# Performance work log

Hardware: AMD Instinct MI355X
Metric: run time of the kernel (lower is better)

Reference implementation:

```python
import jax, jax.numpy as jnp
import numpy as np

N, D, H = 8192, 1280, 16
K = D // H          # head_dim = 80
S = 16              # number of packed segments
L = N // S          # tokens per segment = 512
SCALE = K ** -0.5


def rotate_half(x):
    x1, x2 = jnp.split(x, 2, axis=-1)
    return jnp.concatenate([-x2, x1], axis=-1)


def setup_inputs() -> dict:
    key = jax.random.key(0)
    ks = jax.random.split(key, 4)
    # RoPE tables over head_dim, shared by all heads
    inv_freq = 1.0 / (10000.0 ** (jnp.arange(0, K, 2, dtype=jnp.float32) / K))
    freqs = jnp.outer(jnp.arange(N, dtype=jnp.float32), inv_freq)  # [N, K/2]
    emb = jnp.concatenate([freqs, freqs], axis=-1)                 # [N, K]
    return {
        "hidden_ND": jax.random.normal(ks[0], (N, D), jnp.float32),
        "cu_seqlens": jnp.arange(S + 1, dtype=jnp.int32) * L,      # equal-length segments
        "cos_NK": jnp.cos(emb),
        "sin_NK": jnp.sin(emb),
        "qkv_w": jax.random.normal(ks[1], (D, 3 * D), jnp.float32) * (D ** -0.5),
        "qkv_b": jnp.zeros((3 * D,), jnp.float32),
        "proj_w": jax.random.normal(ks[2], (D, D), jnp.float32) * (D ** -0.5),
        "proj_b": jnp.zeros((D,), jnp.float32),
    }


def reference(hidden_ND, cu_seqlens, cos_NK, sin_NK, qkv_w, qkv_b, proj_w, proj_b):
    n = hidden_ND.shape[0]
    qkv = (hidden_ND @ qkv_w + qkv_b).reshape(n, 3, H, K)
    q, k, v = qkv[:, 0], qkv[:, 1], qkv[:, 2]          # each [N, H, K]
    cos = cos_NK[:, None, :]
    sin = sin_NK[:, None, :]
    q = q * cos + rotate_half(q) * sin
    k = k * cos + rotate_half(k) * sin
    # Block-diagonal attention over equal-length segments defined by cu_seqlens.
    num_seqs = cu_seqlens.shape[0] - 1
    seg_len = n // num_seqs
    qs = q.reshape(num_seqs, seg_len, H, K)
    ks_ = k.reshape(num_seqs, seg_len, H, K)
    vs = v.reshape(num_seqs, seg_len, H, K)
    logits = jnp.einsum('slhk,smhk->shlm', qs, ks_) * SCALE   # [S, H, L, L]
    w = jax.nn.softmax(logits.astype(jnp.float32), axis=-1).astype(logits.dtype)
    out = jnp.einsum('shlm,smhk->slhk', w, vs).reshape(n, H * K)
    return out @ proj_w + proj_b
```

## Files before the change

### kernel.cpp

```cpp
#include <hip/hip_runtime.h>

#define LOG2E 1.44269504088896340736f
#define ATT_SCALE 0.11180339887498949f

typedef _Float16 half8 __attribute__((ext_vector_type(8)));
typedef _Float16 half4v __attribute__((ext_vector_type(4)));
typedef float f32x4 __attribute__((ext_vector_type(4)));

#define MFMA(a, b, c) __builtin_amdgcn_mfma_f32_16x16x32_f16((a), (b), (c), 0, 0, 0)

__device__ __forceinline__ void async16(const _Float16* g, _Float16* l) {
  __builtin_amdgcn_global_load_lds(
      (const __attribute__((address_space(1))) unsigned int*)g,
      (__attribute__((address_space(3))) unsigned int*)l,
      16, 0, 0);
}

__global__ __launch_bounds__(256) void cvt_k(const float* __restrict__ in,
                                             _Float16* __restrict__ out, int n4) {
  int i = blockIdx.x * 256 + threadIdx.x;
  if (i < n4) {
    f32x4 v = ((const f32x4*)in)[i];
    half4v hv;
    hv[0] = (_Float16)v[0]; hv[1] = (_Float16)v[1];
    hv[2] = (_Float16)v[2]; hv[3] = (_Float16)v[3];
    ((half4v*)out)[i] = hv;
  }
}

__global__ __launch_bounds__(256) void transpose_cvt_k(const float* __restrict__ in,
                                                       _Float16* __restrict__ out,
                                                       int R, int C) {
  __shared__ float tile[32][33];
  const int tx = threadIdx.x & 31, ty = threadIdx.x >> 5;
  const int c0 = blockIdx.x * 32, r0 = blockIdx.y * 32;
#pragma unroll
  for (int i = 0; i < 32; i += 8)
    tile[ty + i][tx] = in[(size_t)(r0 + ty + i) * C + c0 + tx];
  __syncthreads();
#pragma unroll
  for (int i = 0; i < 32; i += 8)
    out[(size_t)(c0 + ty + i) * R + r0 + tx] = (_Float16)tile[tx][ty + i];
}

template <int MODE>
__global__ __launch_bounds__(256) void gemm_k(const _Float16* __restrict__ A,
                                              const _Float16* __restrict__ BT,
                                              const float* __restrict__ bias,
                                              _Float16* __restrict__ Qf,
                                              _Float16* __restrict__ Kf,
                                              _Float16* __restrict__ VTf,
                                              float* __restrict__ Out) {
  __shared__ _Float16 sA[128 * 64];
  __shared__ _Float16 sB[128 * 64];
  const int tid = threadIdx.x;
  const int wave = tid >> 6, lane = tid & 63;
  const int quad = lane >> 4, l16 = lane & 15;
  const int m0 = blockIdx.x * 128;
  const int n0 = blockIdx.y * 128;
  const int mw = (wave & 1) * 64, nw = (wave >> 1) * 64;
  const int KD = 1280;

  f32x4 acc[4][4] = {};

  for (int kt = 0; kt < KD; kt += 64) {
#pragma unroll
    for (int c = 0; c < 4; ++c) {
      const int j = wave * 4 + c;
      const int row = j * 8 + (lane >> 3);
      const int srcg = (lane & 7) ^ (row & 7);
      async16(A + (size_t)(m0 + row) * KD + kt + srcg * 8, &sA[j * 512]);
      async16(BT + (size_t)(n0 + row) * KD + kt + srcg * 8, &sB[j * 512]);
    }
    __syncthreads();
#pragma unroll
    for (int ks = 0; ks < 2; ++ks) {
      half8 af[4], bf[4];
#pragma unroll
      for (int i = 0; i < 4; ++i) {
        const int ra = mw + i * 16 + l16;
        const int rb = nw + i * 16 + l16;
        af[i] = *(const half8*)&sA[ra * 64 + (((ks * 4 + quad) ^ (ra & 7)) * 8)];
        bf[i] = *(const half8*)&sB[rb * 64 + (((ks * 4 + quad) ^ (rb & 7)) * 8)];
      }
#pragma unroll
      for (int i = 0; i < 4; ++i)
#pragma unroll
        for (int j2 = 0; j2 < 4; ++j2)
          acc[i][j2] = MFMA(af[i], bf[j2], acc[i][j2]);
    }
    __syncthreads();
  }

#pragma unroll
  for (int i = 0; i < 4; ++i) {
#pragma unroll
    for (int j2 = 0; j2 < 4; ++j2) {
      const int col = n0 + nw + j2 * 16 + l16;
      const float bv = bias[col];
      const int rowb = m0 + mw + i * 16 + quad * 4;
#pragma unroll
      for (int r = 0; r < 4; ++r) {
        const float v = acc[i][j2][r] + bv;
        const int mrow = rowb + r;
        if (MODE == 0) {
          const int which = col / 1280;
          const int rem = col - which * 1280;
          const int h = rem / 80;
          const int kk = rem - h * 80;
          const int s = mrow >> 9, l = mrow & 511;
          const int shh = s * 16 + h;
          if (which == 0)
            Qf[((size_t)shh * 512 + l) * 96 + kk] = (_Float16)v;
          else if (which == 1)
            Kf[((size_t)shh * 512 + l) * 96 + kk] = (_Float16)v;
          else
            VTf[((size_t)shh * 80 + kk) * 512 + l] = (_Float16)v;
        } else {
          Out[(size_t)mrow * 1280 + col] = v;
        }
      }
    }
  }
}

__global__ __launch_bounds__(256) void rope_k(_Float16* __restrict__ Qf,
                                              _Float16* __restrict__ Kf,
                                              const float* __restrict__ cosNK,
                                              const float* __restrict__ sinNK) {
  const int gid = blockIdx.x * 256 + threadIdx.x;
  const int j = gid & 63;
  const int row = gid >> 6;
  const int qk = row >> 17;
  const int r = row & 131071;
  _Float16* buf = qk ? Kf : Qf;
  const int l = r & 511;
  const int s = r >> 13;
  const int t = s * 512 + l;
  const size_t base = (size_t)r * 96;
  if (j < 40) {
    const float v1 = (float)buf[base + j];
    const float v2 = (float)buf[base + j + 40];
    const float c1 = cosNK[t * 80 + j], s1 = sinNK[t * 80 + j];
    const float c2 = cosNK[t * 80 + j + 40], s2 = sinNK[t * 80 + j + 40];
    buf[base + j] = (_Float16)(v1 * c1 - v2 * s1);
    buf[base + j + 40] = (_Float16)(v2 * c2 + v1 * s2);
  } else if (j < 56) {
    buf[base + 40 + j] = (_Float16)0.f;
  }
}

__global__ __launch_bounds__(256) void attn_k(const _Float16* __restrict__ Qf,
                                              const _Float16* __restrict__ Kf,
                                              const _Float16* __restrict__ VTf,
                                              _Float16* __restrict__ attnA) {
  __shared__ _Float16 sQP[128 * 96];
  __shared__ _Float16 sK[64 * 96];
  __shared__ _Float16 sV[96 * 72];
  const int tid = threadIdx.x;
  const int wave = tid >> 6, lane = tid & 63;
  const int quad = lane >> 4, l16 = lane & 15;
  const int shh = blockIdx.x;
  const int qt = blockIdx.y;
  const int h = shh & 15;
  const int s = shh >> 4;

  const _Float16* Qb = Qf + ((size_t)shh * 512 + qt * 128) * 96;
  const _Float16* Kb0 = Kf + (size_t)shh * 512 * 96;
  const _Float16* Vb0 = VTf + (size_t)shh * 80 * 512;

#pragma unroll
  for (int c = 0; c < 6; ++c) {
    const int j = wave + 4 * c;
    async16(Qb + j * 512 + lane * 8, &sQP[j * 512]);
  }
  for (int idx = tid; idx < 16 * 72; idx += 256) sV[80 * 72 + idx] = (_Float16)1.f;
  __syncthreads();

  const _Float16 c1h = (_Float16)(ATT_SCALE * LOG2E);
  half8 qf[2][3];
#pragma unroll
  for (int rt = 0; rt < 2; ++rt)
#pragma unroll
    for (int ks = 0; ks < 3; ++ks) {
      half8 t = *(const half8*)&sQP[(wave * 32 + rt * 16 + l16) * 96 + ks * 32 + quad * 8];
#pragma unroll
      for (int e = 0; e < 8; ++e) t[e] *= c1h;
      qf[rt][ks] = t;
    }

  f32x4 o[2][6] = {};

  for (int kc = 0; kc < 8; ++kc) {
    __syncthreads();
    const _Float16* Kb = Kb0 + (size_t)kc * 64 * 96;
#pragma unroll
    for (int c = 0; c < 3; ++c) {
      const int j = wave + 4 * c;
      async16(Kb + j * 512 + lane * 8, &sK[j * 512]);
    }
#pragma unroll
    for (int c = 0; c < 3; ++c) {
      const int j = wave + 4 * c;
      const int off = j * 1024 + lane * 16;
      const int vrow = off / 144;
      const int colb = off - vrow * 144;
      if (vrow < 80 && colb < 128)
        async16(Vb0 + (size_t)vrow * 512 + kc * 64 + (colb >> 1), &sV[j * 512]);
    }
    __syncthreads();

    f32x4 sacc[2][4] = {};
#pragma unroll
    for (int nt = 0; nt < 4; ++nt) {
#pragma unroll
      for (int ks = 0; ks < 3; ++ks) {
        half8 kb = *(const half8*)&sK[(nt * 16 + l16) * 96 + ks * 32 + quad * 8];
        sacc[0][nt] = MFMA(qf[0][ks], kb, sacc[0][nt]);
        sacc[1][nt] = MFMA(qf[1][ks], kb, sacc[1][nt]);
      }
    }

    _Float16* sP = sQP;
#pragma unroll
    for (int rt = 0; rt < 2; ++rt)
#pragma unroll
      for (int nt = 0; nt < 4; ++nt)
#pragma unroll
        for (int r = 0; r < 4; ++r)
          sP[(wave * 32 + rt * 16 + quad * 4 + r) * 72 + nt * 16 + l16] =
              (_Float16)__builtin_amdgcn_exp2f(sacc[rt][nt][r]);

#pragma unroll
    for (int ks = 0; ks < 2; ++ks) {
      half8 pa[2];
      pa[0] = *(const half8*)&sP[(wave * 32 + 0 + l16) * 72 + ks * 32 + quad * 8];
      pa[1] = *(const half8*)&sP[(wave * 32 + 16 + l16) * 72 + ks * 32 + quad * 8];
#pragma unroll
      for (int ft = 0; ft < 6; ++ft) {
        half8 vb = *(const half8*)&sV[(ft * 16 + l16) * 72 + ks * 32 + quad * 8];
        o[0][ft] = MFMA(pa[0], vb, o[0][ft]);
        o[1][ft] = MFMA(pa[1], vb, o[1][ft]);
      }
    }
  }

#pragma unroll
  for (int rt = 0; rt < 2; ++rt) {
#pragma unroll
    for (int r = 0; r < 4; ++r) {
      const float inv = 1.0f / o[rt][5][r];
      const int token = s * 512 + qt * 128 + wave * 32 + rt * 16 + quad * 4 + r;
#pragma unroll
      for (int ft = 0; ft < 5; ++ft)
        attnA[(size_t)token * 1280 + h * 80 + ft * 16 + l16] =
            (_Float16)(o[rt][ft][r] * inv);
    }
  }
}

extern "C" void kernel_launch(void* const* d_in, const int* in_sizes, int n_in,
                              void* d_out, int out_size, void* d_ws, size_t ws_size,
                              hipStream_t stream) {
  (void)in_sizes; (void)n_in; (void)out_size; (void)ws_size;
  const float* hidden = (const float*)d_in[0];
  const float* cosNK = (const float*)d_in[2];
  const float* sinNK = (const float*)d_in[3];
  const float* qkv_w = (const float*)d_in[4];
  const float* qkv_b = (const float*)d_in[5];
  const float* proj_w = (const float*)d_in[6];
  const float* proj_b = (const float*)d_in[7];
  float* out = (float*)d_out;

  char* ws = (char*)d_ws;
  _Float16* hA    = (_Float16*)(ws);
  _Float16* wT    = (_Float16*)(ws + 20971520);
  _Float16* projT = (_Float16*)(ws + 30801920);
  _Float16* Qf    = (_Float16*)(ws + 34078720);
  _Float16* Kf    = (_Float16*)(ws + 59244544);
  _Float16* VTf   = (_Float16*)(ws + 84410368);
  _Float16* attnA = (_Float16*)(ws + 105381888);

  cvt_k<<<10240, 256, 0, stream>>>(hidden, hA, 2621440);
  transpose_cvt_k<<<dim3(120, 40), 256, 0, stream>>>(qkv_w, wT, 1280, 3840);
  transpose_cvt_k<<<dim3(40, 40), 256, 0, stream>>>(proj_w, projT, 1280, 1280);
  gemm_k<0><<<dim3(64, 30), 256, 0, stream>>>(hA, wT, qkv_b, Qf, Kf, VTf, nullptr);
  rope_k<<<65536, 256, 0, stream>>>(Qf, Kf, cosNK, sinNK);
  attn_k<<<dim3(256, 4), 256, 0, stream>>>(Qf, Kf, VTf, attnA);
  gemm_k<1><<<dim3(64, 10), 256, 0, stream>>>(attnA, projT, proj_b, nullptr, nullptr,
                                              nullptr, out);
}
```

Measured before the change: 389.9 us.

## Shrink GEMM k-tile, pad K smem, transpose QK^T and pack P stores

```diff
diff --git a/kernel.cpp b/kernel.cpp
--- a/kernel.cpp
+++ b/kernel.cpp
@@ -5,6 +5,7 @@
 
 typedef _Float16 half8 __attribute__((ext_vector_type(8)));
 typedef _Float16 half4v __attribute__((ext_vector_type(4)));
+typedef __fp16 fp16x2 __attribute__((ext_vector_type(2)));
 typedef float f32x4 __attribute__((ext_vector_type(4)));
 
 #define MFMA(a, b, c) __builtin_amdgcn_mfma_f32_16x16x32_f16((a), (b), (c), 0, 0, 0)
@@ -51,8 +52,8 @@
                                               _Float16* __restrict__ Kf,
                                               _Float16* __restrict__ VTf,
                                               float* __restrict__ Out) {
-  __shared__ _Float16 sA[128 * 64];
-  __shared__ _Float16 sB[128 * 64];
+  __shared__ _Float16 sA[128 * 32];
+  __shared__ _Float16 sB[128 * 32];
   const int tid = threadIdx.x;
   const int wave = tid >> 6, lane = tid & 63;
   const int quad = lane >> 4, l16 = lane & 15;
@@ -61,34 +62,31 @@
   const int mw = (wave & 1) * 64, nw = (wave >> 1) * 64;
   const int KD = 1280;
 
+  const int srcg = (lane & 3) ^ ((lane >> 3) & 3);
+  const int rg = (quad ^ ((l16 >> 1) & 3)) * 8;
+
   f32x4 acc[4][4] = {};
 
-  for (int kt = 0; kt < KD; kt += 64) {
-#pragma unroll
-    for (int c = 0; c < 4; ++c) {
-      const int j = wave * 4 + c;
-      const int row = j * 8 + (lane >> 3);
-      const int srcg = (lane & 7) ^ (row & 7);
+  for (int kt = 0; kt < KD; kt += 32) {
+#pragma unroll
+    for (int c = 0; c < 2; ++c) {
+      const int j = wave * 2 + c;
+      const int row = j * 16 + (lane >> 2);
       async16(A + (size_t)(m0 + row) * KD + kt + srcg * 8, &sA[j * 512]);
       async16(BT + (size_t)(n0 + row) * KD + kt + srcg * 8, &sB[j * 512]);
     }
     __syncthreads();
-#pragma unroll
-    for (int ks = 0; ks < 2; ++ks) {
-      half8 af[4], bf[4];
-#pragma unroll
-      for (int i = 0; i < 4; ++i) {
-        const int ra = mw + i * 16 + l16;
-        const int rb = nw + i * 16 + l16;
-        af[i] = *(const half8*)&sA[ra * 64 + (((ks * 4 + quad) ^ (ra & 7)) * 8)];
-        bf[i] = *(const half8*)&sB[rb * 64 + (((ks * 4 + quad) ^ (rb & 7)) * 8)];
-      }
-#pragma unroll
-      for (int i = 0; i < 4; ++i)
-#pragma unroll
-        for (int j2 = 0; j2 < 4; ++j2)
-          acc[i][j2] = MFMA(af[i], bf[j2], acc[i][j2]);
-    }
+    half8 af[4], bf[4];
+#pragma unroll
+    for (int i = 0; i < 4; ++i) {
+      af[i] = *(const half8*)&sA[(mw + i * 16 + l16) * 32 + rg];
+      bf[i] = *(const half8*)&sB[(nw + i * 16 + l16) * 32 + rg];
+    }
+#pragma unroll
+    for (int i = 0; i < 4; ++i)
+#pragma unroll
+      for (int j2 = 0; j2 < 4; ++j2)
+        acc[i][j2] = MFMA(af[i], bf[j2], acc[i][j2]);
     __syncthreads();
   }
 
@@ -154,8 +152,8 @@
                                               const _Float16* __restrict__ Kf,
                                               const _Float16* __restrict__ VTf,
                                               _Float16* __restrict__ attnA) {
-  __shared__ _Float16 sQP[128 * 96];
-  __shared__ _Float16 sK[64 * 96];
+  __shared__ _Float16 sP[128 * 72];
+  __shared__ _Float16 sK[64 * 104];
   __shared__ _Float16 sV[96 * 72];
   const int tid = threadIdx.x;
   const int wave = tid >> 6, lane = tid & 63;
@@ -169,35 +167,36 @@
   const _Float16* Kb0 = Kf + (size_t)shh * 512 * 96;
   const _Float16* Vb0 = VTf + (size_t)shh * 80 * 512;
 
-#pragma unroll
-  for (int c = 0; c < 6; ++c) {
-    const int j = wave + 4 * c;
-    async16(Qb + j * 512 + lane * 8, &sQP[j * 512]);
-  }
-  for (int idx = tid; idx < 16 * 72; idx += 256) sV[80 * 72 + idx] = (_Float16)1.f;
-  __syncthreads();
-
   const _Float16 c1h = (_Float16)(ATT_SCALE * LOG2E);
   half8 qf[2][3];
 #pragma unroll
   for (int rt = 0; rt < 2; ++rt)
 #pragma unroll
     for (int ks = 0; ks < 3; ++ks) {
-      half8 t = *(const half8*)&sQP[(wave * 32 + rt * 16 + l16) * 96 + ks * 32 + quad * 8];
+      half8 t = *(const half8*)(Qb + (size_t)(wave * 32 + rt * 16 + l16) * 96 +
+                                ks * 32 + quad * 8);
 #pragma unroll
       for (int e = 0; e < 8; ++e) t[e] *= c1h;
       qf[rt][ks] = t;
     }
 
+  for (int idx = tid; idx < 16 * 72; idx += 256) sV[80 * 72 + idx] = (_Float16)1.f;
+
   f32x4 o[2][6] = {};
 
   for (int kc = 0; kc < 8; ++kc) {
     __syncthreads();
     const _Float16* Kb = Kb0 + (size_t)kc * 64 * 96;
 #pragma unroll
-    for (int c = 0; c < 3; ++c) {
+    for (int c = 0; c < 4; ++c) {
       const int j = wave + 4 * c;
-      async16(Kb + j * 512 + lane * 8, &sK[j * 512]);
+      if (j < 13) {
+        const int off = j * 1024 + lane * 16;
+        const int krow = off / 208;
+        const int kcol = off - krow * 208;
+        if (kcol < 192)
+          async16(Kb + (size_t)krow * 96 + (kcol >> 1), &sK[j * 512]);
+      }
     }
 #pragma unroll
     for (int c = 0; c < 3; ++c) {
@@ -212,24 +211,29 @@
 
     f32x4 sacc[2][4] = {};
 #pragma unroll
-    for (int nt = 0; nt < 4; ++nt) {
+    for (int mt = 0; mt < 4; ++mt) {
 #pragma unroll
       for (int ks = 0; ks < 3; ++ks) {
-        half8 kb = *(const half8*)&sK[(nt * 16 + l16) * 96 + ks * 32 + quad * 8];
-        sacc[0][nt] = MFMA(qf[0][ks], kb, sacc[0][nt]);
-        sacc[1][nt] = MFMA(qf[1][ks], kb, sacc[1][nt]);
-      }
-    }
-
-    _Float16* sP = sQP;
-#pragma unroll
-    for (int rt = 0; rt < 2; ++rt)
-#pragma unroll
-      for (int nt = 0; nt < 4; ++nt)
-#pragma unroll
-        for (int r = 0; r < 4; ++r)
-          sP[(wave * 32 + rt * 16 + quad * 4 + r) * 72 + nt * 16 + l16] =
-              (_Float16)__builtin_amdgcn_exp2f(sacc[rt][nt][r]);
+        half8 kb = *(const half8*)&sK[(mt * 16 + l16) * 104 + ks * 32 + quad * 8];
+        sacc[0][mt] = MFMA(kb, qf[0][ks], sacc[0][mt]);
+        sacc[1][mt] = MFMA(kb, qf[1][ks], sacc[1][mt]);
+      }
+    }
+
+#pragma unroll
+    for (int rt = 0; rt < 2; ++rt) {
+#pragma unroll
+      for (int mt = 0; mt < 4; ++mt) {
+        union { fp16x2 h2[2]; half4v h4; } u;
+        u.h2[0] = __builtin_amdgcn_cvt_pkrtz(
+            __builtin_amdgcn_exp2f(sacc[rt][mt][0]),
+            __builtin_amdgcn_exp2f(sacc[rt][mt][1]));
+        u.h2[1] = __builtin_amdgcn_cvt_pkrtz(
+            __builtin_amdgcn_exp2f(sacc[rt][mt][2]),
+            __builtin_amdgcn_exp2f(sacc[rt][mt][3]));
+        *(half4v*)&sP[(wave * 32 + rt * 16 + l16) * 72 + mt * 16 + quad * 4] = u.h4;
+      }
+    }
 
 #pragma unroll
     for (int ks = 0; ks < 2; ++ks) {
```

After: 372.2 us. -4.5%, faster.
